# Kernel optimization log

Measured on AMD Instinct MI355X. Metric: run time of the kernel, lower is better.

## Reference

```python
import jax, jax.numpy as jnp
import numpy as np

G, R, M, H, NH, OUT = 2048, 1024, 1024, 256, 8, 2
DH = H // NH


def _ln(x, g, b):
    m = jnp.mean(x, -1, keepdims=True)
    v = jnp.var(x, -1, keepdims=True)
    return (x - m) * jax.lax.rsqrt(v + 1e-5) * g + b


def _mha(xq, xkv, w, mask=None):
    # w: [4, H, H] = (Wq, Wk, Wv, Wo); mask: [Nq, Nk] bool (True = attend)
    q = (xq @ w[0]).reshape(-1, NH, DH)
    k = (xkv @ w[1]).reshape(-1, NH, DH)
    v = (xkv @ w[2]).reshape(-1, NH, DH)
    s = jnp.einsum('qhd,khd->hqk', q, k) * np.float32(1.0 / np.sqrt(DH))
    if mask is not None:
        s = jnp.where(mask[None], s, jnp.float32(-1e9))
    a = jax.nn.softmax(s, -1)
    ctx = jnp.einsum('hqk,khd->qhd', a, v).reshape(xq.shape[0], H)
    return ctx @ w[3]


def setup_inputs() -> dict:
    key = jax.random.key(0)
    ks = jax.random.split(key, 32)
    sc = np.float32(1.0 / np.sqrt(H))

    def n(i, shape, s=sc):
        return jax.random.normal(ks[i], shape, jnp.float32) * s

    inp = {}
    inp['gene_emb'] = n(0, (G, H), 0.02)
    inp['reaction_emb'] = n(1, (R, H), 0.02)
    inp['metab_emb'] = n(2, (M, H), 0.02)
    # PreProcessor (note: torch code reuses ONE LayerNorm instance -> shared params)
    inp['pre_w1'] = n(3, (H, H)); inp['pre_b1'] = jnp.zeros((H,), jnp.float32)
    inp['pre_w2'] = n(4, (H, H)); inp['pre_b2'] = jnp.zeros((H,), jnp.float32)
    inp['pre_ln_g'] = jnp.ones((H,), jnp.float32); inp['pre_ln_b'] = jnp.zeros((H,), jnp.float32)
    # NSA: 'M' block = masked attention per edge type (4), 'S' block = full self-attn per node type (3)
    inp['wm'] = n(5, (4, 4, H, H))
    inp['ws'] = n(6, (3, 4, H, H))
    inp['ln_g'] = jnp.ones((3, H), jnp.float32); inp['ln_b'] = jnp.zeros((3, H), jnp.float32)
    # AttentionalGraphAggregation
    inp['gate_w1'] = n(7, (H, H // 2)); inp['gate_b1'] = jnp.zeros((H // 2,), jnp.float32)
    inp['gate_w2'] = n(8, (H // 2, 1)); inp['gate_b2'] = jnp.zeros((1,), jnp.float32)
    inp['tr_w'] = n(9, (H, H)); inp['tr_b'] = jnp.zeros((H,), jnp.float32)
    # prediction head: num_layers=1 -> single Linear
    inp['head_w'] = n(10, (H, OUT)); inp['head_b'] = jnp.zeros((OUT,), jnp.float32)
    # dense edge masks (sparse biological graphs)
    inp['adj_pp'] = jax.random.bernoulli(ks[11], 0.01, (G, G))
    inp['adj_rr'] = jax.random.bernoulli(ks[12], 0.01, (G, G))
    inp['inc_gpr'] = jax.random.bernoulli(ks[13], 0.01, (R, G))
    inp['adj_mm'] = jax.random.bernoulli(ks[14], 0.01, (M, M))
    return inp


def reference(gene_emb, reaction_emb, metab_emb, pre_w1, pre_b1, pre_w2, pre_b2,
              pre_ln_g, pre_ln_b, wm, ws, ln_g, ln_b, gate_w1, gate_b1, gate_w2,
              gate_b2, tr_w, tr_b, head_w, head_b, adj_pp, adj_rr, inc_gpr, adj_mm):
    # preprocessor MLP on gene embeddings (single-graph path; dropout=eval/identity)
    h = jax.nn.relu(_ln(gene_emb @ pre_w1 + pre_b1, pre_ln_g, pre_ln_b))
    xg = jax.nn.relu(_ln(h @ pre_w2 + pre_b2, pre_ln_g, pre_ln_b))
    xr, xm = reaction_emb, metab_emb
    # 'M' block: masked cross/self attention per edge type, sum-aggregated per dst type
    mg = _mha(xg, xg, wm[0], adj_pp) + _mha(xg, xg, wm[1], adj_rr)
    mr = _mha(xr, xg, wm[2], inc_gpr)
    mm = _mha(xm, xm, wm[3], adj_mm)
    xg, xr, xm = xg + mg, xr + mr, xm + mm
    # 'S' block: full self-attention within each node set
    xg = xg + _mha(xg, xg, ws[0])
    xr = xr + _mha(xr, xr, ws[1])
    xm = xm + _mha(xm, xm, ws[2])
    # per-node-type layer norms (gene branch feeds the head)
    xg = _ln(xg, ln_g[0], ln_b[0])
    # attentional graph aggregation over gene nodes (single graph -> plain softmax)
    gate = jax.nn.relu(xg @ gate_w1 + gate_b1) @ gate_w2 + gate_b2  # [G, 1]
    a = jax.nn.softmax(gate, 0)
    t = jax.nn.relu(xg @ tr_w + tr_b)
    pooled = jnp.sum(a * t, 0, keepdims=True)  # [1, H]
    return pooled @ head_w + head_b  # [1, OUT]
```

## Files before the change

### kernel.cpp

```cpp
#include <hip/hip_runtime.h>
#include <hip/hip_bf16.h>
#include <cmath>
#include <cstdint>

typedef unsigned int u32;
typedef unsigned char u8;
typedef unsigned short ushort;
typedef __attribute__((ext_vector_type(8))) short short8;
typedef __attribute__((ext_vector_type(4))) float f32x4;
typedef __attribute__((ext_vector_type(16))) float f32x16;
typedef __attribute__((ext_vector_type(4))) unsigned short us4;

#define Gn 2048
#define Hd 256
#define CSTRIDE 192

static __device__ __forceinline__ ushort f2bf(float x) {
    __hip_bfloat16 b = __float2bfloat16(x);
    return *reinterpret_cast<ushort*>(&b);
}
static __device__ __forceinline__ float bf2f(ushort u) {
    return __uint_as_float(((u32)u) << 16);
}


template <int BETA, int OUTMODE, int QKVMODE, int KT, int LNF, int LNRELU, int WRA>
static __device__ __forceinline__ void gemm_body(
    const int bx, const int by, const int bz,
    const float* __restrict__ A, int lda,
    const ushort* __restrict__ bt_hi, const ushort* __restrict__ bt_lo,
    int slot0, int slot2, const float* __restrict__ bias,
    const float* __restrict__ lng, const float* __restrict__ lnb,
    float* __restrict__ C, int N, float* __restrict__ Aout)
{
    const int tid = threadIdx.x;
    const int wv = tid >> 6, l = tid & 63;
    const int lr = l & 15, lg = l >> 4;
    const int row = bx * 32 + wv * 16 + lr;
    const int col0 = by * 64;
    int slot = slot0, zq = 0, buf = 0;
    if (QKVMODE == 1) { slot = slot0 + bz + bz / 3; zq = bz % 3; buf = bz / 3; }
    else if (QKVMODE == 2) { slot = slot0 + bz; zq = bz; }
    const ushort* bhb = bt_hi + (long)slot * 65536;
    const ushort* blb = bt_lo + (long)slot * 65536;
    const float* arow = A + (long)row * lda;

    float mean = 0.f, rs = 0.f;
    if (LNF) {
        float s = 0.f, s2 = 0.f;
        #pragma unroll
        for (int ks = 0; ks < 8; ++ks) {
            const float4 a0 = *(const float4*)&arow[ks * 32 + lg * 8];
            const float4 a1 = *(const float4*)&arow[ks * 32 + lg * 8 + 4];
            s  += (a0.x + a0.y) + (a0.z + a0.w) + (a1.x + a1.y) + (a1.z + a1.w);
            s2 += a0.x * a0.x + a0.y * a0.y + a0.z * a0.z + a0.w * a0.w +
                  a1.x * a1.x + a1.y * a1.y + a1.z * a1.z + a1.w * a1.w;
        }
        s += __shfl_xor(s, 16);  s += __shfl_xor(s, 32);
        s2 += __shfl_xor(s2, 16); s2 += __shfl_xor(s2, 32);
        mean = s * (1.f / 256.f);
        rs = rsqrtf(s2 * (1.f / 256.f) - mean * mean + 1e-5f);
    }

    const f32x4 z4 = {0.f, 0.f, 0.f, 0.f};
    f32x4 acc[4] = {z4, z4, z4, z4};

    #pragma unroll
    for (int ks = 0; ks < KT / 32; ++ks) {
        const int k0 = ks * 32;
        const ushort* bh; const ushort* bl; int kbi = ks;
        if (KT == 512 && k0 >= 256) {
            bh = bt_hi + (long)slot2 * 65536;
            bl = bt_lo + (long)slot2 * 65536;
            kbi = ks - 8;
        } else { bh = bhb; bl = blb; }
        float av[8];
        *(float4*)&av[0] = *(const float4*)&arow[k0 + lg * 8];
        *(float4*)&av[4] = *(const float4*)&arow[k0 + lg * 8 + 4];
        if (LNF) {
            float gvv[8], bvv[8];
            *(float4*)&gvv[0] = *(const float4*)&lng[k0 + lg * 8];
            *(float4*)&gvv[4] = *(const float4*)&lng[k0 + lg * 8 + 4];
            *(float4*)&bvv[0] = *(const float4*)&lnb[k0 + lg * 8];
            *(float4*)&bvv[4] = *(const float4*)&lnb[k0 + lg * 8 + 4];
            #pragma unroll
            for (int j = 0; j < 8; ++j) {
                float v = (av[j] - mean) * rs * gvv[j] + bvv[j];
                if (LNRELU) v = fmaxf(v, 0.f);
                av[j] = v;
            }
            if (WRA && by == 0 && bz == 0) {
                *(float4*)&Aout[(long)row * 256 + k0 + lg * 8] = *(float4*)&av[0];
                *(float4*)&Aout[(long)row * 256 + k0 + lg * 8 + 4] = *(float4*)&av[4];
            }
        }
        short8 ahi, alo;
        #pragma unroll
        for (int j = 0; j < 8; ++j) {
            const u32 bi = __float_as_uint(av[j]);
            ahi[j] = (short)(bi >> 16);
            const float fh = __uint_as_float(bi & 0xffff0000u);
            alo[j] = (short)f2bf(av[j] - fh);
        }
        #pragma unroll
        for (int f = 0; f < 4; ++f) {
            const long bo = (long)(((by * 4 + f) * 8 + kbi) << 9) + (l << 3);
            const short8 bhi = *(const short8*)&bh[bo];
            const short8 blo = *(const short8*)&bl[bo];
            acc[f] = __builtin_amdgcn_mfma_f32_16x16x32_bf16(ahi, bhi, acc[f], 0, 0, 0);
            acc[f] = __builtin_amdgcn_mfma_f32_16x16x32_bf16(alo, bhi, acc[f], 0, 0, 0);
            acc[f] = __builtin_amdgcn_mfma_f32_16x16x32_bf16(ahi, blo, acc[f], 0, 0, 0);
        }
    }

    const float QS = 0.17677669529663687f * 1.4426950408889634f;

    #pragma unroll
    for (int f = 0; f < 4; ++f) {
        const int col = col0 + f * 16 + lr;
        const float bv = bias ? bias[col] : 0.f;
        #pragma unroll
        for (int r = 0; r < 4; ++r) {
            const int rr = bx * 32 + wv * 16 + lg * 4 + r;
            float v = acc[f][r] + bv;
            if (OUTMODE == 1) {
                if (zq == 0) v *= QS;
                ushort* ob = (ushort*)C + (long)buf * 1572864;
                const int h = col >> 5, d = col & 31;
                if (QKVMODE == 1 || zq < 2)
                    ob[zq * 524288 + ((h * 2048 + rr) << 5) + d] = f2bf(v);
                else
                    ob[1048576 + ((h * 32 + d) << 11) + rr] = f2bf(v);
            } else {
                if (BETA) v += C[(long)rr * N + col];
                C[(long)rr * N + col] = v;
            }
        }
    }
}

__global__ __launch_bounds__(256) void mergedA_kernel(
    const u8* __restrict__ adj, int* __restrict__ det0, int* __restrict__ det1,
    const float* __restrict__ pre_w1, const float* __restrict__ pre_w2,
    const float* __restrict__ wm, const float* __restrict__ wsw,
    const float* __restrict__ gate_w1, const float* __restrict__ tr_w,
    ushort* __restrict__ bt_hi, ushort* __restrict__ bt_lo)
{
    __shared__ float T[32][257];
    __shared__ int sd0[4], sd1[4];
    const int tid = threadIdx.x;
    if (blockIdx.x < 64) {
        const int idx = blockIdx.x * 256 + tid;
        const uint4 w = ((const uint4*)adj)[idx];
        int c0 = ((w.x & 0xffu) ? 1 : 0) + ((w.y & 0xffu) ? 1 : 0) +
                 ((w.z & 0xffu) ? 1 : 0) + ((w.w & 0xffu) ? 1 : 0);
        int c1 = ((w.x & 0xffffff00u) ? 1 : 0) + ((w.y & 0xffffff00u) ? 1 : 0) +
                 ((w.z & 0xffffff00u) ? 1 : 0) + ((w.w & 0xffffff00u) ? 1 : 0);
        #pragma unroll
        for (int o = 1; o < 64; o <<= 1) { c0 += __shfl_xor(c0, o); c1 += __shfl_xor(c1, o); }
        if ((tid & 63) == 0) { sd0[tid >> 6] = c0; sd1[tid >> 6] = c1; }
        __syncthreads();
        if (tid == 0) {
            det0[blockIdx.x] = sd0[0] + sd0[1] + sd0[2] + sd0[3];
            det1[blockIdx.x] = sd1[0] + sd1[1] + sd1[2] + sd1[3];
        }
        return;
    }
    const int b2 = blockIdx.x - 64;
    const int slot = b2 >> 3;
    const int kb = b2 & 7;
    const int k0 = kb * 32;
    const float* src; int ncols = 256;
    if (slot == 0) src = pre_w1;
    else if (slot == 1) src = pre_w2;
    else if (slot < 6) src = wm + (long)(slot - 2) * 65536;
    else if (slot < 10) src = wm + (long)(4 + slot - 6) * 65536;
    else if (slot < 14) src = wsw + (long)(slot - 10) * 65536;
    else if (slot == 14) { src = gate_w1; ncols = 128; }
    else src = tr_w;

    const int lsh = (ncols == 256) ? 6 : 5;
    const int tot = 32 << lsh;
    for (int i = tid; i < tot; i += 256) {
        const int kk = i >> lsh, c4 = (i & ((1 << lsh) - 1)) << 2;
        const float4 v = *(const float4*)&src[(long)(k0 + kk) * ncols + c4];
        T[kk][c4 + 0] = v.x; T[kk][c4 + 1] = v.y;
        T[kk][c4 + 2] = v.z; T[kk][c4 + 3] = v.w;
    }
    __syncthreads();
    if (tid < ncols) {
        ushort hb[32], lb[32];
        #pragma unroll
        for (int kk = 0; kk < 32; ++kk) {
            const float x = T[kk][tid];
            const u32 bi = __float_as_uint(x);
            const ushort h = (ushort)(bi >> 16);
            const float fh = __uint_as_float(bi & 0xffff0000u);
            hb[kk] = h; lb[kk] = f2bf(x - fh);
        }
        const int cb = tid >> 4, lr = tid & 15;
        const long base = (long)slot * 65536 + ((cb * 8 + kb) << 9);
        ushort* oh = bt_hi + base;
        ushort* ol = bt_lo + base;
        #pragma unroll
        for (int lg2 = 0; lg2 < 4; ++lg2) {
            const int off = (lg2 * 16 + lr) << 3;
            *(uint4*)&oh[off] = *(const uint4*)&hb[lg2 * 8];
            *(uint4*)&ol[off] = *(const uint4*)&lb[lg2 * 8];
        }
    }
}

__global__ __launch_bounds__(128) void mergedB_kernel(
    const u8* __restrict__ src0, const u8* __restrict__ src1,
    const int* __restrict__ det0, const int* __restrict__ det1,
    u32* __restrict__ bits,
    const float* __restrict__ gene_emb,
    const ushort* __restrict__ bt_hi, const ushort* __restrict__ bt_lo,
    const float* __restrict__ pre_b1, float* __restrict__ tmp0)
{
    const int tid = threadIdx.x;
    if (blockIdx.x < 2048) {
        const int lane = tid & 63;
        int c0 = det0[lane], c1 = det1[lane];
        #pragma unroll
        for (int o = 1; o < 64; o <<= 1) { c0 += __shfl_xor(c0, o); c1 += __shfl_xor(c1, o); }
        const int f = (c0 > 0) ? ((c1 > 0) ? 1 : 0) : 2;
        const int W = blockIdx.x * 128 + tid;
        const int z = W >> 17;
        const int rem = W & 131071;
        const int row = rem >> 6, w = rem & 63;
        const u8* src = z ? src1 : src0;
        u32 v = 0;
        if (f == 1) {
            const uint4* p = (const uint4*)(src + (long)row * 2048 + w * 32);
            const uint4 q0 = p[0], q1 = p[1];
            const u32 ws8[8] = {q0.x, q0.y, q0.z, q0.w, q1.x, q1.y, q1.z, q1.w};
            #pragma unroll
            for (int j = 0; j < 8; ++j) {
                const u32 x = ws8[j];
                const u32 m = (((x & 0x7f7f7f7fu) + 0x7f7f7f7fu) | x) & 0x80808080u;
                const u32 b4 = ((m >> 7) & 1u) | ((m >> 14) & 2u) |
                               ((m >> 21) & 4u) | ((m >> 28) & 8u);
                v |= b4 << (j * 4);
            }
        } else if (f == 0) {
            const uint4* p = (const uint4*)((const int*)src + (long)row * 2048 + w * 32);
            #pragma unroll
            for (int j = 0; j < 8; ++j) {
                const uint4 q = p[j];
                v |= (q.x ? 1u : 0u) << (j * 4 + 0);
                v |= (q.y ? 1u : 0u) << (j * 4 + 1);
                v |= (q.z ? 1u : 0u) << (j * 4 + 2);
                v |= (q.w ? 1u : 0u) << (j * 4 + 3);
            }
        } else {
            const uint4* p = (const uint4*)((const float*)src + (long)row * 2048 + w * 32);
            #pragma unroll
            for (int j = 0; j < 8; ++j) {
                const uint4 q = p[j];
                v |= ((q.x & 0x7fffffffu) ? 1u : 0u) << (j * 4 + 0);
                v |= ((q.y & 0x7fffffffu) ? 1u : 0u) << (j * 4 + 1);
                v |= ((q.z & 0x7fffffffu) ? 1u : 0u) << (j * 4 + 2);
                v |= ((q.w & 0x7fffffffu) ? 1u : 0u) << (j * 4 + 3);
            }
        }
        bits[(long)z * 131072 + rem] = v;
        return;
    }
    const int b2 = blockIdx.x - 2048;
    gemm_body<0, 0, 0, 256, 0, 0, 0>(b2 >> 2, b2 & 3, 0, gene_emb, 256,
                                     bt_hi, bt_lo, 0, 0, pre_b1,
                                     nullptr, nullptr, tmp0, 256, nullptr);
}

__global__ __launch_bounds__(128) void mergedC_kernel(
    const u32* __restrict__ bits, int* __restrict__ deg, int* __restrict__ colidx,
    const float* __restrict__ tmp0,
    const ushort* __restrict__ bt_hi, const ushort* __restrict__ bt_lo,
    const float* __restrict__ pre_b2, const float* __restrict__ pre_ln_g,
    const float* __restrict__ pre_ln_b, float* __restrict__ tmp1)
{
    if (blockIdx.x < 32) {
        const int flat = blockIdx.x * 128 + threadIdx.x;
        const int z = flat >> 11, r = flat & 2047;
        const u32* b = bits + (long)z * 131072 + r * 64;
        int* ci = colidx + ((long)z * 2048 + r) * CSTRIDE;
        int d = 0;
        for (int w = 0; w < 64; ++w) {
            u32 x = b[w];
            while (x) {
                const int j = __ffs(x) - 1;
                if (d < CSTRIDE) ci[d] = w * 32 + j;
                ++d;
                x &= x - 1;
            }
        }
        deg[z * 2048 + r] = d < CSTRIDE ? d : CSTRIDE;
        return;
    }
    const int b2 = blockIdx.x - 32;
    gemm_body<0, 0, 0, 256, 1, 1, 0>(b2 >> 2, b2 & 3, 0, tmp0, 256,
                                     bt_hi, bt_lo, 1, 0, pre_b2,
                                     pre_ln_g, pre_ln_b, tmp1, 256, nullptr);
}

__global__ __launch_bounds__(128) void qkvm_kernel(
    const float* __restrict__ tmp1,
    const ushort* __restrict__ bt_hi, const ushort* __restrict__ bt_lo,
    const float* __restrict__ pre_ln_g, const float* __restrict__ pre_ln_b,
    float* __restrict__ qkvb, float* __restrict__ xg1)
{
    gemm_body<0, 1, 1, 256, 1, 1, 1>(blockIdx.x, blockIdx.y, blockIdx.z,
                                     tmp1, 256, bt_hi, bt_lo, 2, 0, nullptr,
                                     pre_ln_g, pre_ln_b, qkvb, 256, xg1);
}
__global__ __launch_bounds__(128) void wo_m_kernel(
    const float* __restrict__ ctx2,
    const ushort* __restrict__ bt_hi, const ushort* __restrict__ bt_lo,
    float* __restrict__ xg1)
{
    gemm_body<1, 0, 0, 512, 0, 0, 0>(blockIdx.x, blockIdx.y, 0, ctx2, 512,
                                     bt_hi, bt_lo, 5, 9, nullptr,
                                     nullptr, nullptr, xg1, 256, nullptr);
}
__global__ __launch_bounds__(128) void qkvs_kernel(
    const float* __restrict__ xg1,
    const ushort* __restrict__ bt_hi, const ushort* __restrict__ bt_lo,
    float* __restrict__ qkvb)
{
    gemm_body<0, 1, 2, 256, 0, 0, 0>(blockIdx.x, blockIdx.y, blockIdx.z,
                                     xg1, 256, bt_hi, bt_lo, 10, 0, nullptr,
                                     nullptr, nullptr, qkvb, 256, nullptr);
}
__global__ __launch_bounds__(128) void wo_s_kernel(
    const float* __restrict__ ctx2,
    const ushort* __restrict__ bt_hi, const ushort* __restrict__ bt_lo,
    float* __restrict__ xg1)
{
    gemm_body<1, 0, 0, 256, 0, 0, 0>(blockIdx.x, blockIdx.y, 0, ctx2, 512,
                                     bt_hi, bt_lo, 13, 0, nullptr,
                                     nullptr, nullptr, xg1, 256, nullptr);
}

__global__ __launch_bounds__(64) void attn_sparse_kernel(
    const ushort* __restrict__ qkvb, const int* __restrict__ deg,
    const int* __restrict__ colidx, float* __restrict__ ctx)
{
    const int r = blockIdx.x, z = blockIdx.y;
    const ushort* qb = qkvb + (long)z * 1572864;
    const ushort* kb = qb + 524288;
    const ushort* vr = qb + 1048576;
    const int l = threadIdx.x;
    const int h = l >> 3, dg = l & 7;
    float* orow = &ctx[(long)r * 512 + z * 256 + h * 32 + dg * 4];
    const int n = deg[z * 2048 + r];
    if (n == 0) {
        float a0 = 0.f, a1 = 0.f, a2 = 0.f, a3 = 0.f;
        for (int k = 0; k < 2048; ++k) {
            const us4 vv = *(const us4*)&vr[((h * 2048 + k) << 5) + dg * 4];
            a0 += bf2f(vv[0]); a1 += bf2f(vv[1]); a2 += bf2f(vv[2]); a3 += bf2f(vv[3]);
        }
        float4 o; const float inv = 1.f / 2048.f;
        o.x = a0 * inv; o.y = a1 * inv; o.z = a2 * inv; o.w = a3 * inv;
        *(float4*)orow = o;
        return;
    }
    float q0, q1, q2, q3;
    {
        const us4 qv = *(const us4*)&qb[((h * 2048 + r) << 5) + dg * 4];
        q0 = bf2f(qv[0]); q1 = bf2f(qv[1]); q2 = bf2f(qv[2]); q3 = bf2f(qv[3]);
    }
    const int* ci = colidx + ((long)z * 2048 + r) * CSTRIDE;
    float m = -INFINITY, lsum = 0.f;
    float a0 = 0.f, a1 = 0.f, a2 = 0.f, a3 = 0.f;
    int kn = ci[0];
    us4 kv = *(const us4*)&kb[((h * 2048 + kn) << 5) + dg * 4];
    us4 vv = *(const us4*)&vr[((h * 2048 + kn) << 5) + dg * 4];
    for (int e = 0; e < n; ++e) {
        const us4 kc = kv, vc = vv;
        if (e + 1 < n) {
            kn = ci[e + 1];
            kv = *(const us4*)&kb[((h * 2048 + kn) << 5) + dg * 4];
            vv = *(const us4*)&vr[((h * 2048 + kn) << 5) + dg * 4];
        }
        float s = q0 * bf2f(kc[0]) + q1 * bf2f(kc[1]) +
                  q2 * bf2f(kc[2]) + q3 * bf2f(kc[3]);
        s += __shfl_xor(s, 1); s += __shfl_xor(s, 2); s += __shfl_xor(s, 4);
        const float mn = fmaxf(m, s);
        const float fac = __builtin_amdgcn_exp2f(m - mn);
        const float p = __builtin_amdgcn_exp2f(s - mn);
        lsum = lsum * fac + p;
        a0 = a0 * fac + p * bf2f(vc[0]);
        a1 = a1 * fac + p * bf2f(vc[1]);
        a2 = a2 * fac + p * bf2f(vc[2]);
        a3 = a3 * fac + p * bf2f(vc[3]);
        m = mn;
    }
    const float inv = 1.f / lsum;
    float4 o; o.x = a0 * inv; o.y = a1 * inv; o.z = a2 * inv; o.w = a3 * inv;
    *(float4*)orow = o;
}

__global__ __launch_bounds__(512) void attn_dense_kernel(
    const ushort* __restrict__ qkvb, float* __restrict__ ctx)
{
    const ushort* qb = qkvb;
    const ushort* kb = qb + 524288;
    const ushort* vt = qb + 1048576;
    const int h = blockIdx.x, qt = blockIdx.y;
    const int wv = threadIdx.x >> 6;
    const int l = threadIdx.x & 63;
    const int lq = l & 31;
    const int hi = l >> 5;
    const int qglob = qt * 32 + lq;

    __shared__ float Mm[7][32], Ml[7][32];
    __shared__ float Macc[7][64][16];
    __shared__ float ctile[32][33];

    const int qoff = ((h * 2048 + qglob) << 5) + hi * 8;
    const short8 qf0 = *(const short8*)&qb[qoff];
    const short8 qf1 = *(const short8*)&qb[qoff + 16];

    float m = -INFINITY, lsum = 0.f;
    f32x16 acc, zz16;
    #pragma unroll
    for (int i = 0; i < 16; ++i) { acc[i] = 0.f; zz16[i] = 0.f; }

    const int kt0 = wv * 256;
    #pragma unroll 2
    for (int it = 0; it < 8; ++it) {
        const int kbase = kt0 + it * 32;
        const int koff = ((h * 2048 + kbase + lq) << 5) + hi * 8;
        const short8 kf0 = *(const short8*)&kb[koff];
        const short8 kf1 = *(const short8*)&kb[koff + 16];
        f32x16 s = __builtin_amdgcn_mfma_f32_32x32x16_bf16(kf0, qf0, zz16, 0, 0, 0);
        s = __builtin_amdgcn_mfma_f32_32x32x16_bf16(kf1, qf1, s, 0, 0, 0);
        float sc[16];
        #pragma unroll
        for (int i = 0; i < 16; ++i) sc[i] = s[i];
        float t[8];
        #pragma unroll
        for (int i = 0; i < 8; ++i) t[i] = fmaxf(sc[i], sc[i + 8]);
        #pragma unroll
        for (int i = 0; i < 4; ++i) t[i] = fmaxf(t[i], t[i + 4]);
        float mt = fmaxf(fmaxf(t[0], t[1]), fmaxf(t[2], t[3]));
        mt = fmaxf(mt, __shfl_xor(mt, 32));
        const float mn = fmaxf(m, mt);
        if (__ballot(mn != m)) {
            const float fac = __builtin_amdgcn_exp2f(m - mn);
            lsum *= fac;
            #pragma unroll
            for (int i = 0; i < 16; ++i) acc[i] *= fac;
            m = mn;
        }
        #pragma unroll
        for (int i = 0; i < 16; ++i) sc[i] = __builtin_amdgcn_exp2f(sc[i] - m);
        #pragma unroll
        for (int i = 0; i < 8; ++i) t[i] = sc[i] + sc[i + 8];
        #pragma unroll
        for (int i = 0; i < 4; ++i) t[i] = t[i] + t[i + 4];
        float ps = (t[0] + t[1]) + (t[2] + t[3]);
        ps += __shfl_xor(ps, 32);
        lsum += ps;
        u32 pk[8];
        #pragma unroll
        for (int g = 0; g < 4; ++g) {
            asm("v_cvt_pk_bf16_f32 %0, %1, %2"
                : "=v"(pk[2 * g]) : "v"(sc[4 * g + 0]), "v"(sc[4 * g + 1]));
            asm("v_cvt_pk_bf16_f32 %0, %1, %2"
                : "=v"(pk[2 * g + 1]) : "v"(sc[4 * g + 2]), "v"(sc[4 * g + 3]));
        }
        asm volatile("v_permlane32_swap_b32 %0, %1" : "+v"(pk[0]), "+v"(pk[2]));
        asm volatile("v_permlane32_swap_b32 %0, %1" : "+v"(pk[1]), "+v"(pk[3]));
        asm volatile("v_permlane32_swap_b32 %0, %1" : "+v"(pk[4]), "+v"(pk[6]));
        asm volatile("v_permlane32_swap_b32 %0, %1" : "+v"(pk[5]), "+v"(pk[7]));
        short8 pB0, pB1;
        ((u32*)&pB0)[0] = pk[0]; ((u32*)&pB0)[1] = pk[1];
        ((u32*)&pB0)[2] = pk[2]; ((u32*)&pB0)[3] = pk[3];
        ((u32*)&pB1)[0] = pk[4]; ((u32*)&pB1)[1] = pk[5];
        ((u32*)&pB1)[2] = pk[6]; ((u32*)&pB1)[3] = pk[7];
        const int voff = ((h * 32 + lq) << 11) + kbase + hi * 8;
        const short8 vf0 = *(const short8*)&vt[voff];
        const short8 vf1 = *(const short8*)&vt[voff + 16];
        acc = __builtin_amdgcn_mfma_f32_32x32x16_bf16(vf0, pB0, acc, 0, 0, 0);
        acc = __builtin_amdgcn_mfma_f32_32x32x16_bf16(vf1, pB1, acc, 0, 0, 0);
    }

    if (wv) {
        if (l < 32) { Mm[wv - 1][l] = m; Ml[wv - 1][l] = lsum; }
        #pragma unroll
        for (int i = 0; i < 16; ++i) Macc[wv - 1][l][i] = acc[i];
    }
    __syncthreads();
    if (wv == 0) {
        float M = m;
        #pragma unroll
        for (int w = 0; w < 7; ++w) M = fmaxf(M, Mm[w][lq]);
        const float f0 = __builtin_amdgcn_exp2f(m - M);
        float den = lsum * f0;
        float o[16];
        #pragma unroll
        for (int i = 0; i < 16; ++i) o[i] = acc[i] * f0;
        #pragma unroll
        for (int w = 0; w < 7; ++w) {
            const float fw = __builtin_amdgcn_exp2f(Mm[w][lq] - M);
            den += Ml[w][lq] * fw;
            #pragma unroll
            for (int i = 0; i < 16; ++i) o[i] += Macc[w][l][i] * fw;
        }
        const float inv = 1.f / den;
        #pragma unroll
        for (int i = 0; i < 16; ++i)
            ctile[(i & 3) + 8 * (i >> 2) + 4 * hi][lq] = o[i] * inv;
    }
    __syncthreads();
    if (threadIdx.x < 256) {
        const int t = threadIdx.x;
        const int q = t >> 3, d0 = (t & 7) << 2;
        float4 ov;
        ov.x = ctile[d0 + 0][q]; ov.y = ctile[d0 + 1][q];
        ov.z = ctile[d0 + 2][q]; ov.w = ctile[d0 + 3][q];
        *(float4*)&ctx[(long)(qt * 32 + q) * 512 + h * 32 + d0] = ov;
    }
}

__global__ __launch_bounds__(64) void aggr_gemm_kernel(
    const float* __restrict__ xg1,
    const ushort* __restrict__ bt_hi, const ushort* __restrict__ bt_lo,
    const float* __restrict__ ln_g, const float* __restrict__ ln_b,
    const float* __restrict__ tr_b, const float* __restrict__ g_b1,
    const float* __restrict__ g_w2, const float* __restrict__ g_b2,
    float* __restrict__ t_out, float* __restrict__ gv)
{
    const int l = threadIdx.x;
    const int lr = l & 15, lg = l >> 4;
    const int row0 = blockIdx.x * 16;
    const int gate = (blockIdx.y == 8);
    const int slot = gate ? 14 : 15;
    const int col0 = gate ? 0 : blockIdx.y * 32;
    const int NF = gate ? 8 : 2;
    const ushort* bh0 = bt_hi + (long)slot * 65536;
    const ushort* bl0 = bt_lo + (long)slot * 65536;
    const float* arow = xg1 + (long)(row0 + lr) * 256;

    float s = 0.f, s2 = 0.f;
    #pragma unroll
    for (int ks = 0; ks < 8; ++ks) {
        const float4 a0 = *(const float4*)&arow[ks * 32 + lg * 8];
        const float4 a1 = *(const float4*)&arow[ks * 32 + lg * 8 + 4];
        s  += (a0.x + a0.y) + (a0.z + a0.w) + (a1.x + a1.y) + (a1.z + a1.w);
        s2 += a0.x * a0.x + a0.y * a0.y + a0.z * a0.z + a0.w * a0.w +
              a1.x * a1.x + a1.y * a1.y + a1.z * a1.z + a1.w * a1.w;
    }
    s += __shfl_xor(s, 16);  s += __shfl_xor(s, 32);
    s2 += __shfl_xor(s2, 16); s2 += __shfl_xor(s2, 32);
    const float mean = s * (1.f / 256.f);
    const float rs = rsqrtf(s2 * (1.f / 256.f) - mean * mean + 1e-5f);

    const f32x4 z4 = {0.f, 0.f, 0.f, 0.f};
    f32x4 acc[8] = {z4, z4, z4, z4, z4, z4, z4, z4};

    #pragma unroll
    for (int ks = 0; ks < 8; ++ks) {
        const int k0 = ks * 32;
        float av[8], gvv[8], bvv[8];
        *(float4*)&av[0] = *(const float4*)&arow[k0 + lg * 8];
        *(float4*)&av[4] = *(const float4*)&arow[k0 + lg * 8 + 4];
        *(float4*)&gvv[0] = *(const float4*)&ln_g[k0 + lg * 8];
        *(float4*)&gvv[4] = *(const float4*)&ln_g[k0 + lg * 8 + 4];
        *(float4*)&bvv[0] = *(const float4*)&ln_b[k0 + lg * 8];
        *(float4*)&bvv[4] = *(const float4*)&ln_b[k0 + lg * 8 + 4];
        short8 ahi, alo;
        #pragma unroll
        for (int j = 0; j < 8; ++j) {
            const float vn = (av[j] - mean) * rs * gvv[j] + bvv[j];
            const u32 bi = __float_as_uint(vn);
            ahi[j] = (short)(bi >> 16);
            const float fh = __uint_as_float(bi & 0xffff0000u);
            alo[j] = (short)f2bf(vn - fh);
        }
        for (int f = 0; f < NF; ++f) {
            const int cb = gate ? f : ((int)blockIdx.y * 2 + f);
            const long bo = (long)((cb * 8 + ks) << 9) + (l << 3);
            const short8 bhi = *(const short8*)&bh0[bo];
            const short8 blo = *(const short8*)&bl0[bo];
            acc[f] = __builtin_amdgcn_mfma_f32_16x16x32_bf16(ahi, bhi, acc[f], 0, 0, 0);
            acc[f] = __builtin_amdgcn_mfma_f32_16x16x32_bf16(alo, bhi, acc[f], 0, 0, 0);
            acc[f] = __builtin_amdgcn_mfma_f32_16x16x32_bf16(ahi, blo, acc[f], 0, 0, 0);
        }
    }

    if (!gate) {
        #pragma unroll
        for (int f = 0; f < 2; ++f) {
            const int col = col0 + f * 16 + lr;
            const float bv = tr_b[col];
            #pragma unroll
            for (int r = 0; r < 4; ++r) {
                const int rr = row0 + lg * 4 + r;
                t_out[(long)rr * 256 + col] = fmaxf(acc[f][r] + bv, 0.f);
            }
        }
    } else {
        float b1v[8], w2v[8];
        #pragma unroll
        for (int f = 0; f < 8; ++f) {
            b1v[f] = g_b1[f * 16 + lr];
            w2v[f] = g_w2[f * 16 + lr];
        }
        const float b2 = g_b2[0];
        #pragma unroll
        for (int r = 0; r < 4; ++r) {
            float t = 0.f;
            #pragma unroll
            for (int f = 0; f < 8; ++f)
                t += fmaxf(acc[f][r] + b1v[f], 0.f) * w2v[f];
            #pragma unroll
            for (int o = 1; o < 16; o <<= 1) t += __shfl_xor(t, o);
            if (lr == 0) gv[row0 + lg * 4 + r] = t + b2;
        }
    }
}

__global__ __launch_bounds__(256) void wsum_part_kernel(
    const float* __restrict__ gv, const float* __restrict__ t,
    float* __restrict__ partial, float* __restrict__ denp, float* __restrict__ mpart)
{
    const float L2E = 1.4426950408889634f;
    const int b = blockIdx.x, tid = threadIdx.x;
    float M = -INFINITY;
    #pragma unroll
    for (int i = 0; i < 32; ++i) M = fmaxf(M, gv[b * 32 + i]);
    float s = 0.f, den = 0.f;
    #pragma unroll 4
    for (int i = 0; i < 32; ++i) {
        const int r = b * 32 + i;
        const float w = __builtin_amdgcn_exp2f((gv[r] - M) * L2E);
        den += w;
        s += w * t[(long)r * 256 + tid];
    }
    partial[b * 256 + tid] = s;
    if (tid == 0) { denp[b] = den; mpart[b] = M; }
}

__global__ __launch_bounds__(256) void head2_kernel(
    const float* __restrict__ partial, const float* __restrict__ denp,
    const float* __restrict__ mpart, const float* __restrict__ hw,
    const float* __restrict__ hb, float* __restrict__ out)
{
    __shared__ float fb[64];
    __shared__ float dtot;
    __shared__ float red0[4], red1[4];
    const float L2E = 1.4426950408889634f;
    const int tid = threadIdx.x;
    if (tid < 64) {
        const float mb = mpart[tid];
        float M = mb;
        #pragma unroll
        for (int o = 1; o < 64; o <<= 1) M = fmaxf(M, __shfl_xor(M, o));
        const float f = __builtin_amdgcn_exp2f((mb - M) * L2E);
        fb[tid] = f;
        float dv = f * denp[tid];
        #pragma unroll
        for (int o = 1; o < 64; o <<= 1) dv += __shfl_xor(dv, o);
        if (tid == 0) dtot = dv;
    }
    __syncthreads();
    float p = 0.f;
    #pragma unroll 8
    for (int b = 0; b < 64; ++b) p += fb[b] * partial[b * 256 + tid];
    p /= dtot;
    float s0 = p * hw[tid * 2 + 0];
    float s1 = p * hw[tid * 2 + 1];
    #pragma unroll
    for (int o = 1; o < 64; o <<= 1) { s0 += __shfl_xor(s0, o); s1 += __shfl_xor(s1, o); }
    if ((tid & 63) == 0) { red0[tid >> 6] = s0; red1[tid >> 6] = s1; }
    __syncthreads();
    if (tid == 0) {
        out[0] = red0[0] + red0[1] + red0[2] + red0[3] + hb[0];
        out[1] = red1[0] + red1[1] + red1[2] + red1[3] + hb[1];
    }
}

extern "C" void kernel_launch(void* const* d_in, const int* in_sizes, int n_in,
                              void* d_out, int out_size, void* d_ws, size_t ws_size,
                              hipStream_t stream)
{
    (void)in_sizes; (void)n_in; (void)out_size; (void)ws_size;
    const float* gene_emb = (const float*)d_in[0];
    const float* pre_w1   = (const float*)d_in[3];
    const float* pre_b1   = (const float*)d_in[4];
    const float* pre_w2   = (const float*)d_in[5];
    const float* pre_b2   = (const float*)d_in[6];
    const float* pre_ln_g = (const float*)d_in[7];
    const float* pre_ln_b = (const float*)d_in[8];
    const float* wm       = (const float*)d_in[9];
    const float* wsw      = (const float*)d_in[10];
    const float* ln_g     = (const float*)d_in[11];
    const float* ln_b     = (const float*)d_in[12];
    const float* gate_w1  = (const float*)d_in[13];
    const float* gate_b1  = (const float*)d_in[14];
    const float* gate_w2  = (const float*)d_in[15];
    const float* gate_b2  = (const float*)d_in[16];
    const float* tr_w     = (const float*)d_in[17];
    const float* tr_b     = (const float*)d_in[18];
    const float* head_w   = (const float*)d_in[19];
    const float* head_b   = (const float*)d_in[20];
    const u8* adj_pp      = (const u8*)d_in[21];
    const u8* adj_rr      = (const u8*)d_in[22];

    const long NHf = (long)Gn * Hd;
    float* tmp0    = (float*)d_ws;
    float* tmp1    = tmp0 + NHf;
    float* xg1     = tmp1 + NHf;
    float* ctx2    = xg1 + NHf;
    float* gv      = ctx2 + 2 * NHf;
    float* partial = gv + Gn;
    float* denp    = partial + 64 * 256;
    float* mpart   = denp + 64;
    int* det0      = (int*)(mpart + 64);
    int* det1      = det0 + 64;
    int* deg       = det1 + 64;
    int* colidx    = deg + 4096;
    u32* bits      = (u32*)(colidx + 2L * 2048 * CSTRIDE);
    ushort* qkvb   = (ushort*)(bits + 262144);
    ushort* bt_hi  = qkvb + 2L * 1572864;
    ushort* bt_lo  = bt_hi + 16L * 65536;

    dim3 B256(256), B128(128), T64(64);

    mergedA_kernel<<<dim3(192), B256, 0, stream>>>(adj_pp, det0, det1,
        pre_w1, pre_w2, wm, wsw, gate_w1, tr_w, bt_hi, bt_lo);
    mergedB_kernel<<<dim3(2304), B128, 0, stream>>>(adj_pp, adj_rr, det0, det1,
        bits, gene_emb, bt_hi, bt_lo, pre_b1, tmp0);
    mergedC_kernel<<<dim3(288), B128, 0, stream>>>(bits, deg, colidx, tmp0,
        bt_hi, bt_lo, pre_b2, pre_ln_g, pre_ln_b, tmp1);
    qkvm_kernel<<<dim3(64, 4, 6), B128, 0, stream>>>(tmp1, bt_hi, bt_lo,
        pre_ln_g, pre_ln_b, (float*)qkvb, xg1);
    attn_sparse_kernel<<<dim3(2048, 2), T64, 0, stream>>>(qkvb, deg, colidx, ctx2);
    wo_m_kernel<<<dim3(64, 4), B128, 0, stream>>>(ctx2, bt_hi, bt_lo, xg1);
    qkvs_kernel<<<dim3(64, 4, 3), B128, 0, stream>>>(xg1, bt_hi, bt_lo, (float*)qkvb);
    attn_dense_kernel<<<dim3(8, 64), dim3(512), 0, stream>>>(qkvb, ctx2);
    wo_s_kernel<<<dim3(64, 4), B128, 0, stream>>>(ctx2, bt_hi, bt_lo, xg1);
    aggr_gemm_kernel<<<dim3(128, 9), T64, 0, stream>>>(xg1, bt_hi, bt_lo,
        ln_g, ln_b, tr_b, gate_b1, gate_w2, gate_b2, tmp0, gv);
    wsum_part_kernel<<<dim3(64), B256, 0, stream>>>(gv, tmp0, partial, denp, mpart);
    head2_kernel<<<dim3(1), B256, 0, stream>>>(partial, denp, mpart, head_w, head_b, (float*)d_out);
}
```

Baseline: 191.8 us.

## Fuse CSR build into bitmask kernel, parallelize attention merge, fold head into wsum

Moves the per-row column-index extraction from mergedC into mergedB, so each 128-thread block builds the CSR lists for its own two rows from shared memory. mergedC now runs only the GEMM. The dense attention combine step now spreads the cross-wave softmax merge over all threads instead of leaving it to wave 0, with a padded Macc array. The final head kernel is merged into wsum through an atomic last-block ticket, which removes one launch; the ticket is reset in the first kernel. The CSR extraction now runs serially on 2 threads per block, which may be slower per row than before.

```diff
diff --git a/kernel.cpp b/kernel.cpp
--- a/kernel.cpp
+++ b/kernel.cpp
@@ -144,11 +144,13 @@
     const float* __restrict__ pre_w1, const float* __restrict__ pre_w2,
     const float* __restrict__ wm, const float* __restrict__ wsw,
     const float* __restrict__ gate_w1, const float* __restrict__ tr_w,
-    ushort* __restrict__ bt_hi, ushort* __restrict__ bt_lo)
+    ushort* __restrict__ bt_hi, ushort* __restrict__ bt_lo,
+    u32* __restrict__ ticket)
 {
     __shared__ float T[32][257];
     __shared__ int sd0[4], sd1[4];
     const int tid = threadIdx.x;
+    if (blockIdx.x == 0 && tid == 0) *ticket = 0;
     if (blockIdx.x < 64) {
         const int idx = blockIdx.x * 256 + tid;
         const uint4 w = ((const uint4*)adj)[idx];
@@ -214,11 +216,12 @@
 __global__ __launch_bounds__(128) void mergedB_kernel(
     const u8* __restrict__ src0, const u8* __restrict__ src1,
     const int* __restrict__ det0, const int* __restrict__ det1,
-    u32* __restrict__ bits,
+    u32* __restrict__ bits, int* __restrict__ deg, int* __restrict__ colidx,
     const float* __restrict__ gene_emb,
     const ushort* __restrict__ bt_hi, const ushort* __restrict__ bt_lo,
     const float* __restrict__ pre_b1, float* __restrict__ tmp0)
 {
+    __shared__ u32 sw[128];
     const int tid = threadIdx.x;
     if (blockIdx.x < 2048) {
         const int lane = tid & 63;
@@ -266,6 +269,25 @@
             }
         }
         bits[(long)z * 131072 + rem] = v;
+        sw[tid] = v;
+        __syncthreads();
+        if (tid < 2) {
+            const int rem0 = (blockIdx.x * 128) & 131071;
+            const int r = (rem0 >> 6) + tid;
+            int* ci = colidx + ((long)z * 2048 + r) * CSTRIDE;
+            int d = 0;
+            #pragma unroll 4
+            for (int ww = 0; ww < 64; ++ww) {
+                u32 x = sw[tid * 64 + ww];
+                while (x) {
+                    const int j = __ffs(x) - 1;
+                    if (d < CSTRIDE) ci[d] = ww * 32 + j;
+                    ++d;
+                    x &= x - 1;
+                }
+            }
+            deg[z * 2048 + r] = d < CSTRIDE ? d : CSTRIDE;
+        }
         return;
     }
     const int b2 = blockIdx.x - 2048;
@@ -275,31 +297,12 @@
 }
 
 __global__ __launch_bounds__(128) void mergedC_kernel(
-    const u32* __restrict__ bits, int* __restrict__ deg, int* __restrict__ colidx,
     const float* __restrict__ tmp0,
     const ushort* __restrict__ bt_hi, const ushort* __restrict__ bt_lo,
     const float* __restrict__ pre_b2, const float* __restrict__ pre_ln_g,
     const float* __restrict__ pre_ln_b, float* __restrict__ tmp1)
 {
-    if (blockIdx.x < 32) {
-        const int flat = blockIdx.x * 128 + threadIdx.x;
-        const int z = flat >> 11, r = flat & 2047;
-        const u32* b = bits + (long)z * 131072 + r * 64;
-        int* ci = colidx + ((long)z * 2048 + r) * CSTRIDE;
-        int d = 0;
-        for (int w = 0; w < 64; ++w) {
-            u32 x = b[w];
-            while (x) {
-                const int j = __ffs(x) - 1;
-                if (d < CSTRIDE) ci[d] = w * 32 + j;
-                ++d;
-                x &= x - 1;
-            }
-        }
-        deg[z * 2048 + r] = d < CSTRIDE ? d : CSTRIDE;
-        return;
-    }
-    const int b2 = blockIdx.x - 32;
+    const int b2 = blockIdx.x;
     gemm_body<0, 0, 0, 256, 1, 1, 0>(b2 >> 2, b2 & 3, 0, tmp0, 256,
                                      bt_hi, bt_lo, 1, 0, pre_b2,
                                      pre_ln_g, pre_ln_b, tmp1, 256, nullptr);
@@ -415,8 +418,8 @@
     const int hi = l >> 5;
     const int qglob = qt * 32 + lq;
 
-    __shared__ float Mm[7][32], Ml[7][32];
-    __shared__ float Macc[7][64][16];
+    __shared__ float Mm[8][32], Ml[8][32];
+    __shared__ float Macc[8][64][17];
     __shared__ float ctile[32][33];
 
     const int qoff = ((h * 2048 + qglob) << 5) + hi * 8;
@@ -488,32 +491,33 @@
         acc = __builtin_amdgcn_mfma_f32_32x32x16_bf16(vf1, pB1, acc, 0, 0, 0);
     }
 
-    if (wv) {
-        if (l < 32) { Mm[wv - 1][l] = m; Ml[wv - 1][l] = lsum; }
-        #pragma unroll
-        for (int i = 0; i < 16; ++i) Macc[wv - 1][l][i] = acc[i];
-    }
+    if (l < 32) { Mm[wv][l] = m; Ml[wv][l] = lsum; }
+    #pragma unroll
+    for (int i = 0; i < 16; ++i) Macc[wv][l][i] = acc[i];
     __syncthreads();
-    if (wv == 0) {
-        float M = m;
-        #pragma unroll
-        for (int w = 0; w < 7; ++w) M = fmaxf(M, Mm[w][lq]);
-        const float f0 = __builtin_amdgcn_exp2f(m - M);
-        float den = lsum * f0;
-        float o[16];
-        #pragma unroll
-        for (int i = 0; i < 16; ++i) o[i] = acc[i] * f0;
-        #pragma unroll
-        for (int w = 0; w < 7; ++w) {
-            const float fw = __builtin_amdgcn_exp2f(Mm[w][lq] - M);
-            den += Ml[w][lq] * fw;
-            #pragma unroll
-            for (int i = 0; i < 16; ++i) o[i] += Macc[w][l][i] * fw;
+    {
+        const int t = threadIdx.x;
+        const int q = t & 31, j = t >> 5;
+        float M = Mm[0][q];
+        #pragma unroll
+        for (int w = 1; w < 8; ++w) M = fmaxf(M, Mm[w][q]);
+        float fw[8], den = 0.f;
+        #pragma unroll
+        for (int w = 0; w < 8; ++w) {
+            fw[w] = __builtin_amdgcn_exp2f(Mm[w][q] - M);
+            den += Ml[w][q] * fw[w];
         }
         const float inv = 1.f / den;
         #pragma unroll
-        for (int i = 0; i < 16; ++i)
-            ctile[(i & 3) + 8 * (i >> 2) + 4 * hi][lq] = o[i] * inv;
+        for (int half = 0; half < 2; ++half) {
+            const int d = j + 16 * half;
+            const int i = (d & 3) | ((d >> 3) << 2);
+            const int h2 = (d >> 2) & 1;
+            float o = 0.f;
+            #pragma unroll
+            for (int w = 0; w < 8; ++w) o += Macc[w][h2 * 32 + q][i] * fw[w];
+            ctile[d][q] = o * inv;
+        }
     }
     __syncthreads();
     if (threadIdx.x < 256) {
@@ -624,9 +628,11 @@
     }
 }
 
-__global__ __launch_bounds__(256) void wsum_part_kernel(
+__global__ __launch_bounds__(256) void wsum_head_kernel(
     const float* __restrict__ gv, const float* __restrict__ t,
-    float* __restrict__ partial, float* __restrict__ denp, float* __restrict__ mpart)
+    float* __restrict__ partial, float* __restrict__ denp, float* __restrict__ mpart,
+    const float* __restrict__ hw, const float* __restrict__ hb,
+    float* __restrict__ out, u32* __restrict__ ticket)
 {
     const float L2E = 1.4426950408889634f;
     const int b = blockIdx.x, tid = threadIdx.x;
@@ -643,24 +649,23 @@
     }
     partial[b * 256 + tid] = s;
     if (tid == 0) { denp[b] = den; mpart[b] = M; }
-}
-
-__global__ __launch_bounds__(256) void head2_kernel(
-    const float* __restrict__ partial, const float* __restrict__ denp,
-    const float* __restrict__ mpart, const float* __restrict__ hw,
-    const float* __restrict__ hb, float* __restrict__ out)
-{
+    __threadfence();
+    __syncthreads();
+    __shared__ int lastFlag;
+    if (tid == 0) lastFlag = (atomicAdd(ticket, 1u) == 63u) ? 1 : 0;
+    __syncthreads();
+    if (!lastFlag) return;
+    __threadfence();
+
     __shared__ float fb[64];
     __shared__ float dtot;
     __shared__ float red0[4], red1[4];
-    const float L2E = 1.4426950408889634f;
-    const int tid = threadIdx.x;
     if (tid < 64) {
         const float mb = mpart[tid];
-        float M = mb;
-        #pragma unroll
-        for (int o = 1; o < 64; o <<= 1) M = fmaxf(M, __shfl_xor(M, o));
-        const float f = __builtin_amdgcn_exp2f((mb - M) * L2E);
+        float Mg = mb;
+        #pragma unroll
+        for (int o = 1; o < 64; o <<= 1) Mg = fmaxf(Mg, __shfl_xor(Mg, o));
+        const float f = __builtin_amdgcn_exp2f((mb - Mg) * L2E);
         fb[tid] = f;
         float dv = f * denp[tid];
         #pragma unroll
@@ -670,7 +675,7 @@
     __syncthreads();
     float p = 0.f;
     #pragma unroll 8
-    for (int b = 0; b < 64; ++b) p += fb[b] * partial[b * 256 + tid];
+    for (int bb = 0; bb < 64; ++bb) p += fb[bb] * partial[bb * 256 + tid];
     p /= dtot;
     float s0 = p * hw[tid * 2 + 0];
     float s1 = p * hw[tid * 2 + 1];
@@ -722,7 +727,8 @@
     float* mpart   = denp + 64;
     int* det0      = (int*)(mpart + 64);
     int* det1      = det0 + 64;
-    int* deg       = det1 + 64;
+    u32* ticket    = (u32*)(det1 + 64);
+    int* deg       = (int*)(ticket + 64);
     int* colidx    = deg + 4096;
     u32* bits      = (u32*)(colidx + 2L * 2048 * CSTRIDE);
     ushort* qkvb   = (ushort*)(bits + 262144);
@@ -732,11 +738,11 @@
     dim3 B256(256), B128(128), T64(64);
 
     mergedA_kernel<<<dim3(192), B256, 0, stream>>>(adj_pp, det0, det1,
-        pre_w1, pre_w2, wm, wsw, gate_w1, tr_w, bt_hi, bt_lo);
+        pre_w1, pre_w2, wm, wsw, gate_w1, tr_w, bt_hi, bt_lo, ticket);
     mergedB_kernel<<<dim3(2304), B128, 0, stream>>>(adj_pp, adj_rr, det0, det1,
-        bits, gene_emb, bt_hi, bt_lo, pre_b1, tmp0);
-    mergedC_kernel<<<dim3(288), B128, 0, stream>>>(bits, deg, colidx, tmp0,
-        bt_hi, bt_lo, pre_b2, pre_ln_g, pre_ln_b, tmp1);
+        bits, deg, colidx, gene_emb, bt_hi, bt_lo, pre_b1, tmp0);
+    mergedC_kernel<<<dim3(256), B128, 0, stream>>>(tmp0, bt_hi, bt_lo,
+        pre_b2, pre_ln_g, pre_ln_b, tmp1);
     qkvm_kernel<<<dim3(64, 4, 6), B128, 0, stream>>>(tmp1, bt_hi, bt_lo,
         pre_ln_g, pre_ln_b, (float*)qkvb, xg1);
     attn_sparse_kernel<<<dim3(2048, 2), T64, 0, stream>>>(qkvb, deg, colidx, ctx2);
@@ -746,6 +752,6 @@
     wo_s_kernel<<<dim3(64, 4), B128, 0, stream>>>(ctx2, bt_hi, bt_lo, xg1);
     aggr_gemm_kernel<<<dim3(128, 9), T64, 0, stream>>>(xg1, bt_hi, bt_lo,
         ln_g, ln_b, tr_b, gate_b1, gate_w2, gate_b2, tmp0, gv);
-    wsum_part_kernel<<<dim3(64), B256, 0, stream>>>(gv, tmp0, partial, denp, mpart);
-    head2_kernel<<<dim3(1), B256, 0, stream>>>(partial, denp, mpart, head_w, head_b, (float*)d_out);
-}
+    wsum_head_kernel<<<dim3(64), B256, 0, stream>>>(gv, tmp0, partial, denp,
+        mpart, head_w, head_b, (float*)d_out, ticket);
+}
```

Result: faster. 186.1 us, median of 2 (-2.9%).
